# Optimization experiments

Measured on AMD Instinct MI355X. Metric: run time of the kernel, lower is better.

Reference implementation:

```python
import jax, jax.numpy as jnp
import numpy as np

C = 256  # num_feat

def _maxpool2x2(x):
    B, C_, H, W = x.shape
    return x.reshape(B, C_, H // 2, 2, W // 2, 2).max(axis=(3, 5))

def setup_inputs() -> dict:
    key = jax.random.key(0)
    ks = jax.random.split(key, 6)
    B, H, W = 16, 64, 64
    x = jax.random.normal(ks[0], (B, C, H, W), dtype=jnp.float32)
    s = 1.0 / np.sqrt(C)
    wf = jax.random.normal(ks[1], (C >> 3, C), dtype=jnp.float32) * s
    wg = jax.random.normal(ks[2], (C >> 3, C), dtype=jnp.float32) * s
    wh = jax.random.normal(ks[3], (C >> 1, C), dtype=jnp.float32) * s
    wo = jax.random.normal(ks[4], (C, C >> 1), dtype=jnp.float32) * (1.0 / np.sqrt(C >> 1))
    gamma = jax.random.normal(ks[5], (), dtype=jnp.float32) * 0.1
    return {"x": x, "wf": wf, "wg": wg, "wh": wh, "wo": wo, "gamma": gamma}

def reference(x, wf, wg, wh, wo, gamma):
    B, _, H, W = x.shape
    # 1x1 convs as channel contractions
    f = jnp.einsum('oc,bchw->bohw', wf, x)                 # [B, C/8, H, W]
    g = _maxpool2x2(jnp.einsum('oc,bchw->bohw', wg, x))    # [B, C/8, H/2, W/2]
    h = _maxpool2x2(jnp.einsum('oc,bchw->bohw', wh, x))    # [B, C/2, H/2, W/2]
    f = f.reshape(B, C >> 3, H * W)
    g = g.reshape(B, C >> 3, (H * W) >> 2)
    h = h.reshape(B, C >> 1, (H * W) >> 2)
    # unscaled attention: [B, HW, HW/4]
    beta = jax.nn.softmax(jnp.einsum('bcn,bcm->bnm', f, g), axis=-1)
    att = jnp.einsum('bcm,bnm->bcn', h, beta).reshape(B, C >> 1, H, W)
    o = jnp.einsum('oc,bchw->bohw', wo, att)               # [B, C, H, W]
    return gamma * o + x
```

## Files before the change

### kernel.cpp

```cpp
#include <hip/hip_runtime.h>

#define N_  4096
#define M_  1024

typedef short bf16x8 __attribute__((ext_vector_type(8)));
typedef float f32x4  __attribute__((ext_vector_type(4)));

#define MFMA16(A,B,C) __builtin_amdgcn_mfma_f32_16x16x32_bf16(A,B,C,0,0,0)

__device__ __forceinline__ unsigned short f2b(float f){
    union { float f; unsigned u; } v; v.f = f;
    unsigned r = v.u + 0x7FFFu + ((v.u >> 16) & 1u);
    return (unsigned short)(r >> 16);
}
__device__ __forceinline__ unsigned packbf(float lo, float hi){
    return (unsigned)f2b(lo) | ((unsigned)f2b(hi) << 16);
}

__global__ __launch_bounds__(256)
void k0_wcvt(const float* __restrict__ wf, const float* __restrict__ wg,
             const float* __restrict__ wh, short* __restrict__ wsB) {
    const int i4 = (blockIdx.x * 256 + threadIdx.x) * 4;
    const float* src = (i4 < 8192) ? (wf + i4) : (i4 < 16384) ? (wg + (i4 - 8192))
                                               : (wh + (i4 - 16384));
    float4 v = *(const float4*)src;
    uint2 o; o.x = packbf(v.x, v.y); o.y = packbf(v.z, v.w);
    *(uint2*)(wsB + i4) = o;
}

__global__ __launch_bounds__(512, 2)
void k1_proj(const float* __restrict__ x, const short* __restrict__ wsB,
             const float* __restrict__ wo,
             short* __restrict__ fT, short* __restrict__ gT,
             short* __restrict__ hM, short* __restrict__ woB) {
    __shared__ __align__(64) char sm[65536];
    const int t    = threadIdx.x;
    const int b    = blockIdx.x >> 5;
    const int rp   = blockIdx.x & 31;
    const int nb   = rp * 128;
    const int mb   = rp * 32;
    const int lane = t & 63;
    const int w    = t >> 6;
    const int lr   = lane & 15, lg = lane >> 4;

    {
        const int p   = t & 127;
        const int seg = t >> 7;
        const float* xr0 = x + ((size_t)(b * 256 + 2 * p)) * N_ + nb + seg * 32;
        const float* xr1 = xr0 + N_;
#pragma unroll
        for (int jj = 0; jj < 32; jj += 4) {
            float4 a = *(const float4*)(xr0 + jj);
            float4 c = *(const float4*)(xr1 + jj);
            const float av[4] = {a.x, a.y, a.z, a.w};
            const float cv[4] = {c.x, c.y, c.z, c.w};
#pragma unroll
            for (int e = 0; e < 4; ++e) {
                const int n = seg * 32 + jj + e;
                *(unsigned*)(sm + ((n * 512 + 4 * p) ^ ((n & 7) << 4))) = packbf(av[e], cv[e]);
            }
        }
    }
    if (blockIdx.x < 64) {
        const int i = blockIdx.x * 512 + t;
        woB[i] = (short)f2b(wo[i]);
    }
    __syncthreads();

    bf16x8 xA[8];
#pragma unroll
    for (int kc = 0; kc < 8; ++kc) {
        const int n = w * 16 + lr;
        xA[kc] = *(const bf16x8*)(sm + ((n * 512 + (kc * 32 + lg * 8) * 2) ^ ((n & 7) << 4)));
    }
    f32x4 acc[12];
#pragma unroll
    for (int ot = 0; ot < 12; ++ot) {
        acc[ot] = (f32x4){0.f, 0.f, 0.f, 0.f};
        const short* wrow = wsB + (size_t)(ot * 16 + lr) * 256 + lg * 8;
#pragma unroll
        for (int kc = 0; kc < 8; ++kc) {
            bf16x8 wB = *(const bf16x8*)(wrow + kc * 32);
            acc[ot] = MFMA16(xA[kc], wB, acc[ot]);
        }
    }
    __syncthreads();

#pragma unroll
    for (int ot = 0; ot < 12; ++ot) {
        const int o = ot * 16 + lr;
        const int n = w * 16 + lg * 4;
        const int base = o * 256 + n * 2;
        *(unsigned*)(sm + ((base)     ^ ((o & 7) << 4))) = packbf(acc[ot][0], acc[ot][1]);
        *(unsigned*)(sm + ((base + 4) ^ ((o & 7) << 4))) = packbf(acc[ot][2], acc[ot][3]);
    }
    __syncthreads();

    {
        const int n = t & 127, oq = t >> 7;
        unsigned pk[4];
#pragma unroll
        for (int v = 0; v < 4; ++v) {
            const int o0 = oq * 8 + v * 2;
            unsigned short b0 = *(unsigned short*)(sm + (((o0)     * 256 + n * 2) ^ (((o0)     & 7) << 4)));
            unsigned short b1 = *(unsigned short*)(sm + (((o0 + 1) * 256 + n * 2) ^ (((o0 + 1) & 7) << 4)));
            pk[v] = (unsigned)b0 | ((unsigned)b1 << 16);
        }
        *(uint4*)(fT + ((size_t)(b * N_ + nb + n)) * 32 + oq * 8) = make_uint4(pk[0], pk[1], pk[2], pk[3]);
    }

    {
        const int j  = t & 31;
        const int ob = t >> 5;
#pragma unroll
        for (int i = 0; i < 10; ++i) {
            const int oo = ob + i * 16;
            const int ro = 32 + oo;
            const int base = ro * 256;
            const unsigned u0 = *(unsigned*)(sm + ((base + 4 * j)       ^ ((ro & 7) << 4)));
            const unsigned u1 = *(unsigned*)(sm + ((base + 128 + 4 * j) ^ ((ro & 7) << 4)));
            union { unsigned u; float f; } c0, c1, c2, c3;
            c0.u = u0 << 16; c1.u = u0 & 0xFFFF0000u;
            c2.u = u1 << 16; c3.u = u1 & 0xFFFF0000u;
            const float mx = fmaxf(fmaxf(c0.f, c1.f), fmaxf(c2.f, c3.f));
            if (oo < 32) {
                *(unsigned short*)(sm + 49664 + j * 68 + oo * 2) = f2b(mx);
            } else {
                hM[((size_t)(b * 128 + (oo - 32))) * M_ + mb + j] = (short)f2b(mx);
            }
        }
    }
    __syncthreads();
    if (t < 128) {
        const int jm = t >> 2, q = t & 3;
        const char* pgb = sm + 49664 + jm * 68 + q * 16;
        unsigned v0 = *(unsigned*)(pgb + 0), v1 = *(unsigned*)(pgb + 4),
                 v2 = *(unsigned*)(pgb + 8), v3 = *(unsigned*)(pgb + 12);
        *(uint4*)(gT + ((size_t)(b * M_ + mb + jm)) * 32 + q * 8) = make_uint4(v0, v1, v2, v3);
    }
}

__global__ __launch_bounds__(256, 2)
void k2_attn(const short* __restrict__ fT, const short* __restrict__ gT,
             const short* __restrict__ hM, const short* __restrict__ woB,
             const float* __restrict__ x, const float* __restrict__ gam,
             float* __restrict__ out) {
    __shared__ __align__(64) char sm[49152];
    const int t    = threadIdx.x;
    const int lane = t & 63;
    const int w    = t >> 6;
    const int lr   = lane & 15, lg = lane >> 4;
    const int b    = blockIdx.x >> 6;
    const int nt   = blockIdx.x & 63;
    const int n0   = nt * 64;

    const f32x4 z4 = (f32x4){0.f, 0.f, 0.f, 0.f};

    const bf16x8 fB = *(const bf16x8*)(fT + ((size_t)(b * N_ + n0 + w * 16 + lr)) * 32 + lg * 8);

    f32x4 acc[8];
#pragma unroll
    for (int j = 0; j < 8; ++j) acc[j] = z4;
    float M = -1e30f, Lp = 0.f;

    const int pbase = 32768 + w * 4096;
    const int swz   = (lr & 7) << 4;

    for (int mt8 = 0; mt8 < 8; ++mt8) {
        const int m0 = mt8 * 128;
        __syncthreads();
        {
            bf16x8 hv[8];
#pragma unroll
            for (int i = 0; i < 8; ++i) {
                const int slot = t + i * 256, c = slot >> 4, p = slot & 15;
                hv[i] = *(const bf16x8*)(hM + ((size_t)(b * 128 + c)) * M_ + m0 + p * 8);
            }
#pragma unroll
            for (int i = 0; i < 8; ++i) {
                const int slot = t + i * 256, c = slot >> 4, p = slot & 15;
                *(bf16x8*)(sm + ((c * 256 + p * 16) ^ ((c & 7) << 4))) = hv[i];
            }
        }
        f32x4 s[8];
#pragma unroll
        for (int mt = 0; mt < 8; ++mt) {
            bf16x8 gA = *(const bf16x8*)(gT + ((size_t)(b * M_ + m0 + mt * 16 + lr)) * 32 + lg * 8);
            s[mt] = MFMA16(gA, fB, z4);
        }
        float pm = -1e30f;
#pragma unroll
        for (int mt = 0; mt < 8; ++mt)
            pm = fmaxf(pm, fmaxf(fmaxf(s[mt][0], s[mt][1]), fmaxf(s[mt][2], s[mt][3])));
        pm = fmaxf(pm, __shfl_xor(pm, 16));
        pm = fmaxf(pm, __shfl_xor(pm, 32));
        const float Mn = fmaxf(M, pm);
        const float scale = __expf(M - Mn);
        M = Mn;
        float ps = 0.f;
#pragma unroll
        for (int mt = 0; mt < 8; ++mt) {
#pragma unroll
            for (int r = 0; r < 4; ++r) {
                const float p = __expf(s[mt][r] - Mn);
                s[mt][r] = p; ps += p;
            }
        }
        Lp = Lp * scale + ps;
#pragma unroll
        for (int mt = 0; mt < 8; ++mt) {
            const int base = lr * 256 + (mt * 16 + lg * 4) * 2;
            *(unsigned*)(sm + pbase + ((base)     ^ swz)) = packbf(s[mt][0], s[mt][1]);
            *(unsigned*)(sm + pbase + ((base + 4) ^ swz)) = packbf(s[mt][2], s[mt][3]);
        }
        const float sc0 = __shfl(scale, lg * 4 + 0);
        const float sc1 = __shfl(scale, lg * 4 + 1);
        const float sc2 = __shfl(scale, lg * 4 + 2);
        const float sc3 = __shfl(scale, lg * 4 + 3);
#pragma unroll
        for (int cj = 0; cj < 8; ++cj) {
            acc[cj][0] *= sc0; acc[cj][1] *= sc1; acc[cj][2] *= sc2; acc[cj][3] *= sc3;
        }
        __syncthreads();
#pragma unroll
        for (int kc = 0; kc < 4; ++kc) {
            const bf16x8 pA = *(const bf16x8*)(sm + pbase + ((lr * 256 + (kc * 32 + lg * 8) * 2) ^ swz));
#pragma unroll
            for (int cj = 0; cj < 8; ++cj) {
                const int c = cj * 16 + lr;
                const bf16x8 hB = *(const bf16x8*)(sm + ((c * 256 + (kc * 32 + lg * 8) * 2) ^ ((c & 7) << 4)));
                acc[cj] = MFMA16(pA, hB, acc[cj]);
            }
        }
    }
    Lp += __shfl_xor(Lp, 16);
    Lp += __shfl_xor(Lp, 32);
    const float inv = 1.f / Lp;
    const float iv0 = __shfl(inv, lg * 4 + 0), iv1 = __shfl(inv, lg * 4 + 1),
                iv2 = __shfl(inv, lg * 4 + 2), iv3 = __shfl(inv, lg * 4 + 3);
    __syncthreads();
#pragma unroll
    for (int cj = 0; cj < 8; ++cj) {
        const int c = cj * 16 + lr;
        const float vv[4] = {acc[cj][0] * iv0, acc[cj][1] * iv1, acc[cj][2] * iv2, acc[cj][3] * iv3};
#pragma unroll
        for (int r = 0; r < 4; ++r) {
            const int n = w * 16 + lg * 4 + r;
            *(unsigned short*)(sm + ((n * 256 + c * 2) ^ ((n & 7) << 4))) = f2b(vv[r]);
        }
    }
    __syncthreads();
    const float gamma = gam[0];
#pragma unroll
    for (int ti = 0; ti < 4; ++ti) {
        const int oc0 = w * 64 + ti * 16;
        bf16x8 wA[4];
#pragma unroll
        for (int kc = 0; kc < 4; ++kc)
            wA[kc] = *(const bf16x8*)(woB + (size_t)(oc0 + lr) * 128 + kc * 32 + lg * 8);
#pragma unroll
        for (int ni = 0; ni < 4; ++ni) {
            f32x4 e = z4;
#pragma unroll
            for (int kc = 0; kc < 4; ++kc) {
                const int n = ni * 16 + lr;
                const bf16x8 oB = *(const bf16x8*)(sm + ((n * 256 + (kc * 32 + lg * 8) * 2) ^ swz));
                e = MFMA16(wA[kc], oB, e);
            }
#pragma unroll
            for (int r = 0; r < 4; ++r) {
                const int oc = oc0 + lg * 4 + r;
                const size_t idx = ((size_t)(b * 256 + oc)) * N_ + n0 + ni * 16 + lr;
                out[idx] = gamma * e[r] + x[idx];
            }
        }
    }
}

extern "C" void kernel_launch(void* const* d_in, const int* in_sizes, int n_in,
                              void* d_out, int out_size, void* d_ws, size_t ws_size,
                              hipStream_t stream) {
    (void)in_sizes; (void)n_in; (void)out_size; (void)ws_size;
    const float* x   = (const float*)d_in[0];
    const float* wf  = (const float*)d_in[1];
    const float* wg  = (const float*)d_in[2];
    const float* wh  = (const float*)d_in[3];
    const float* wo  = (const float*)d_in[4];
    const float* gam = (const float*)d_in[5];
    float* out = (float*)d_out;

    short* ws  = (short*)d_ws;
    short* wsB = ws;
    short* woB = ws + 49152;
    short* fT  = ws + 81920;
    short* gT  = ws + 2179072;
    short* hM  = ws + 2703360;

    k0_wcvt<<<dim3(48),   dim3(256), 0, stream>>>(wf, wg, wh, wsB);
    k1_proj<<<dim3(512),  dim3(512), 0, stream>>>(x, wsB, wo, fT, gT, hM, woB);
    k2_attn<<<dim3(1024), dim3(256), 0, stream>>>(fT, gT, hM, woB, x, gam, out);
}
```

Before: 230.6 us.

## Split projection K loop in halves and prefetch next attention tiles into registers

The projection kernel now stages x in two 128-channel halves. The global loads for the second half are issued before the MFMAs on the first half, so load latency overlaps compute and the LDS footprint per stage shrinks. The attention kernel software-pipelines its g and h tile loads into registers one iteration ahead, and both kernels raise their launch_bounds occupancy hints (512,4 and 256,3). The higher occupancy targets could cap registers and cause spills, and the prefetch registers add pressure.

```diff
diff --git a/kernel.cpp b/kernel.cpp
--- a/kernel.cpp
+++ b/kernel.cpp
@@ -28,7 +28,7 @@
     *(uint2*)(wsB + i4) = o;
 }
 
-__global__ __launch_bounds__(512, 2)
+__global__ __launch_bounds__(512, 4)
 void k1_proj(const float* __restrict__ x, const short* __restrict__ wsB,
              const float* __restrict__ wo,
              short* __restrict__ fT, short* __restrict__ gT,
@@ -43,45 +43,82 @@
     const int w    = t >> 6;
     const int lr   = lane & 15, lg = lane >> 4;
 
-    {
-        const int p   = t & 127;
-        const int seg = t >> 7;
-        const float* xr0 = x + ((size_t)(b * 256 + 2 * p)) * N_ + nb + seg * 32;
-        const float* xr1 = xr0 + N_;
-#pragma unroll
-        for (int jj = 0; jj < 32; jj += 4) {
-            float4 a = *(const float4*)(xr0 + jj);
-            float4 c = *(const float4*)(xr1 + jj);
-            const float av[4] = {a.x, a.y, a.z, a.w};
-            const float cv[4] = {c.x, c.y, c.z, c.w};
-#pragma unroll
-            for (int e = 0; e < 4; ++e) {
-                const int n = seg * 32 + jj + e;
-                *(unsigned*)(sm + ((n * 512 + 4 * p) ^ ((n & 7) << 4))) = packbf(av[e], cv[e]);
-            }
-        }
+    const int p5  = t & 63;
+    const int n0s = (t >> 6) * 16;
+    const float* xb = x + ((size_t)(b * 256)) * N_ + nb + n0s;
+
+    float4 r0[4], r1[4];
+#pragma unroll
+    for (int q = 0; q < 4; ++q) {
+        r0[q] = *(const float4*)(xb + (size_t)(2 * p5)     * N_ + q * 4);
+        r1[q] = *(const float4*)(xb + (size_t)(2 * p5 + 1) * N_ + q * 4);
     }
     if (blockIdx.x < 64) {
         const int i = blockIdx.x * 512 + t;
         woB[i] = (short)f2b(wo[i]);
     }
-    __syncthreads();
-
-    bf16x8 xA[8];
-#pragma unroll
-    for (int kc = 0; kc < 8; ++kc) {
+#pragma unroll
+    for (int q = 0; q < 4; ++q) {
+        const float a0[4] = {r0[q].x, r0[q].y, r0[q].z, r0[q].w};
+        const float a1[4] = {r1[q].x, r1[q].y, r1[q].z, r1[q].w};
+#pragma unroll
+        for (int e = 0; e < 4; ++e) {
+            const int n = n0s + q * 4 + e;
+            *(unsigned*)(sm + ((n * 256 + 4 * p5) ^ ((n & 7) << 4))) = packbf(a0[e], a1[e]);
+        }
+    }
+    __syncthreads();
+
+#pragma unroll
+    for (int q = 0; q < 4; ++q) {
+        r0[q] = *(const float4*)(xb + (size_t)(128 + 2 * p5) * N_ + q * 4);
+        r1[q] = *(const float4*)(xb + (size_t)(129 + 2 * p5) * N_ + q * 4);
+    }
+
+    f32x4 acc[12];
+#pragma unroll
+    for (int ot = 0; ot < 12; ++ot) acc[ot] = (f32x4){0.f, 0.f, 0.f, 0.f};
+    {
         const int n = w * 16 + lr;
-        xA[kc] = *(const bf16x8*)(sm + ((n * 512 + (kc * 32 + lg * 8) * 2) ^ ((n & 7) << 4)));
-    }
-    f32x4 acc[12];
-#pragma unroll
-    for (int ot = 0; ot < 12; ++ot) {
-        acc[ot] = (f32x4){0.f, 0.f, 0.f, 0.f};
-        const short* wrow = wsB + (size_t)(ot * 16 + lr) * 256 + lg * 8;
-#pragma unroll
-        for (int kc = 0; kc < 8; ++kc) {
-            bf16x8 wB = *(const bf16x8*)(wrow + kc * 32);
-            acc[ot] = MFMA16(xA[kc], wB, acc[ot]);
+        bf16x8 xA[4];
+#pragma unroll
+        for (int kc = 0; kc < 4; ++kc)
+            xA[kc] = *(const bf16x8*)(sm + ((n * 256 + (kc * 32 + lg * 8) * 2) ^ ((n & 7) << 4)));
+#pragma unroll
+        for (int ot = 0; ot < 12; ++ot) {
+            const short* wrow = wsB + (size_t)(ot * 16 + lr) * 256 + lg * 8;
+#pragma unroll
+            for (int kc = 0; kc < 4; ++kc) {
+                bf16x8 wB = *(const bf16x8*)(wrow + kc * 32);
+                acc[ot] = MFMA16(xA[kc], wB, acc[ot]);
+            }
+        }
+    }
+#pragma unroll
+    for (int q = 0; q < 4; ++q) {
+        const float a0[4] = {r0[q].x, r0[q].y, r0[q].z, r0[q].w};
+        const float a1[4] = {r1[q].x, r1[q].y, r1[q].z, r1[q].w};
+#pragma unroll
+        for (int e = 0; e < 4; ++e) {
+            const int n = n0s + q * 4 + e;
+            *(unsigned*)(sm + 32768 + ((n * 256 + 4 * p5) ^ ((n & 7) << 4))) = packbf(a0[e], a1[e]);
+        }
+    }
+    __syncthreads();
+    {
+        const int n = w * 16 + lr;
+        bf16x8 xA[4];
+#pragma unroll
+        for (int kc = 0; kc < 4; ++kc)
+            xA[kc] = *(const bf16x8*)(sm + 32768 + ((n * 256 + (kc * 32 + lg * 8) * 2) ^ ((n & 7) << 4)));
+#pragma unroll
+        for (int ot = 0; ot < 12; ++ot) {
+            const short* wrow = wsB + (size_t)(ot * 16 + lr) * 256 + 128 + lg * 8;
+#pragma unroll
+            for (int kc = 0; kc < 4; ++kc) {
+                bf16x8 wB = *(const bf16x8*)(wrow + kc * 32);
+                acc[ot] = MFMA16(xA[kc], wB, acc[ot]);
+            }
         }
     }
     __syncthreads();
@@ -140,7 +177,7 @@
     }
 }
 
-__global__ __launch_bounds__(256, 2)
+__global__ __launch_bounds__(256, 3)
 void k2_attn(const short* __restrict__ fT, const short* __restrict__ gT,
              const short* __restrict__ hM, const short* __restrict__ woB,
              const float* __restrict__ x, const float* __restrict__ gam,
@@ -166,27 +203,43 @@
     const int pbase = 32768 + w * 4096;
     const int swz   = (lr & 7) << 4;
 
+    const short* gA0   = gT + ((size_t)(b * M_) + lr) * 32 + lg * 8;
+    const int    hslc  = (t >> 4);
+    const int    hslp  = (t & 15);
+    const short* hMb   = hM + (size_t)(b * 128) * M_;
+
+    bf16x8 gv[8], hv[8];
+#pragma unroll
+    for (int mt = 0; mt < 8; ++mt)
+        gv[mt] = *(const bf16x8*)(gA0 + (size_t)(mt * 16) * 32);
+#pragma unroll
+    for (int i = 0; i < 8; ++i) {
+        const int c = hslc + i * 16;
+        hv[i] = *(const bf16x8*)(hMb + (size_t)c * M_ + hslp * 8);
+    }
+
     for (int mt8 = 0; mt8 < 8; ++mt8) {
         const int m0 = mt8 * 128;
         __syncthreads();
-        {
-            bf16x8 hv[8];
+#pragma unroll
+        for (int i = 0; i < 8; ++i) {
+            const int c = hslc + i * 16;
+            *(bf16x8*)(sm + ((c * 256 + hslp * 16) ^ ((c & 7) << 4))) = hv[i];
+        }
+        f32x4 s[8];
+#pragma unroll
+        for (int mt = 0; mt < 8; ++mt)
+            s[mt] = MFMA16(gv[mt], fB, z4);
+        if (mt8 < 7) {
+            const int m1 = m0 + 128;
+#pragma unroll
+            for (int mt = 0; mt < 8; ++mt)
+                gv[mt] = *(const bf16x8*)(gA0 + (size_t)(m1 + mt * 16) * 32);
 #pragma unroll
             for (int i = 0; i < 8; ++i) {
-                const int slot = t + i * 256, c = slot >> 4, p = slot & 15;
-                hv[i] = *(const bf16x8*)(hM + ((size_t)(b * 128 + c)) * M_ + m0 + p * 8);
-            }
-#pragma unroll
-            for (int i = 0; i < 8; ++i) {
-                const int slot = t + i * 256, c = slot >> 4, p = slot & 15;
-                *(bf16x8*)(sm + ((c * 256 + p * 16) ^ ((c & 7) << 4))) = hv[i];
-            }
-        }
-        f32x4 s[8];
-#pragma unroll
-        for (int mt = 0; mt < 8; ++mt) {
-            bf16x8 gA = *(const bf16x8*)(gT + ((size_t)(b * M_ + m0 + mt * 16 + lr)) * 32 + lg * 8);
-            s[mt] = MFMA16(gA, fB, z4);
+                const int c = hslc + i * 16;
+                hv[i] = *(const bf16x8*)(hMb + (size_t)c * M_ + m1 + hslp * 8);
+            }
         }
         float pm = -1e30f;
 #pragma unroll
```

New measurement: 345.6 us. 1.5x slower.
